# Kernel optimization log

Measured on AMD Instinct MI355X. Metric: run time of the kernel, lower is better.

Reference implementation:

```python
import jax, jax.numpy as jnp
import numpy as np

HID = 512
HEADS = 8
HD = HID // HEADS  # 64


def setup_inputs() -> dict:
    key = jax.random.key(0)
    ks = jax.random.split(key, 16)
    B, LQ, LK = 2, 384, 384
    s_in = 1.0 / np.sqrt(HID)
    s_hd = 1.0 / np.sqrt(HD)
    return {
        "query": jax.random.normal(ks[0], (B, LQ, HID), jnp.float32),
        "key":   jax.random.normal(ks[1], (B, LK, HID), jnp.float32),
        "value": jax.random.normal(ks[2], (B, LK, HID), jnp.float32),
        # linear weights stored as (in, out) so y = x @ W + b
        "Wq": jax.random.uniform(ks[3], (HID, HID), jnp.float32, -s_in, s_in),
        "bq": jnp.zeros((HID,), jnp.float32),
        "Wk": jax.random.uniform(ks[4], (HID, HID), jnp.float32, -s_in, s_in),
        "bk": jnp.zeros((HID,), jnp.float32),
        "Wv": jax.random.uniform(ks[5], (HID, HID), jnp.float32, -s_in, s_in),
        "bv": jnp.zeros((HID,), jnp.float32),
        "Ww": jax.random.uniform(ks[6], (HD, HD), jnp.float32, -s_hd, s_hd),
        "bw": jnp.zeros((HD,), jnp.float32),
        "Wu": jax.random.uniform(ks[7], (HD, HD), jnp.float32, -s_hd, s_hd),
        "bu": jnp.zeros((HD,), jnp.float32),
        "vv": jax.random.uniform(ks[8], (HD,), jnp.float32, -s_hd, s_hd),
        "Wo": jax.random.uniform(ks[9], (HID, HID), jnp.float32, -s_in, s_in),
        "bo": jnp.zeros((HID,), jnp.float32),
    }


def reference(query, key, value, Wq, bq, Wk, bk, Wv, bv, Ww, bw, Wu, bu, vv, Wo, bo):
    B, LQ, _ = query.shape
    LK = key.shape[1]
    scale = jnp.sqrt(jnp.asarray(HD, query.dtype))

    def split_heads(x, L):
        return x.reshape(B, L, HEADS, HD).transpose(0, 2, 1, 3)  # [B,H,L,hd]

    Q = split_heads(query @ Wq + bq, LQ)
    K = split_heads(key @ Wk + bk, LK)
    V = split_heads(value @ Wv + bv, LK)

    qW = Q @ Ww + bw            # [B,H,Lq,hd]
    kU = K @ Wu + bu            # [B,H,Lk,hd]
    # additive energy: tanh(W(Q)+U(K)) . vv  -> [B,H,Lq,Lk]
    e = jnp.tanh(qW[:, :, :, None, :] + kU[:, :, None, :, :])  # [B,H,Lq,Lk,hd]
    energy = jnp.einsum('bhqkd,d->bhqk', e, vv) / scale

    attention = jax.nn.softmax(energy, axis=-1)
    x = jnp.einsum('bhqk,bhkd->bhqd', attention, V)
    x = x.transpose(0, 2, 1, 3).reshape(B, LQ, HID)
    x = x @ Wo + bo
    return (x, attention)
```

## Files before the change

kernel.cpp:

```cpp
#include <hip/hip_runtime.h>

#define HID 512
#define HEADS 8
#define HD 64
#define BATCH 2
#define SEQ 384
#define MROWS (BATCH * SEQ)
#define KT_N 48
#define APACK_S8 (48 * KT_N * 64)
#define BPACK_S8 (32 * KT_N * 64)

#define C1 2.8853900817779268f
#define SSCL 0.18033688011112043f

typedef __attribute__((ext_vector_type(8))) short s8v;
typedef __attribute__((ext_vector_type(4))) float f4v;

__device__ __forceinline__ unsigned short bf16_rne(float x) {
    union { float f; unsigned u; } v; v.f = x;
    unsigned r = v.u + 0x7FFFu + ((v.u >> 16) & 1u);
    return (unsigned short)(r >> 16);
}
__device__ __forceinline__ float bf16_val(unsigned short h) {
    union { float f; unsigned u; } v; v.u = ((unsigned)h) << 16; return v.f;
}

__device__ __forceinline__ void pack_a_one(const float* __restrict__ src,
                                           s8v* __restrict__ dst, int rem)
{
    int g = rem & 63, m = rem >> 6;
    const float4* sp = (const float4*)(src + (size_t)m * HID + g * 8);
    float4 v0 = sp[0], v1 = sp[1];
    float vals[8] = {v0.x, v0.y, v0.z, v0.w, v1.x, v1.y, v1.z, v1.w};
    s8v hi, lo;
    #pragma unroll
    for (int j = 0; j < 8; ++j) {
        unsigned short h = bf16_rne(vals[j]);
        hi[j] = (short)h;
        lo[j] = (short)bf16_rne(vals[j] - bf16_val(h));
    }
    int mt = m >> 4, kt = g >> 2;
    int lanei = (m & 15) | ((g & 3) << 4);
    size_t base = ((size_t)mt * KT_N) * 64 + lanei;
    dst[base + (size_t)kt * 64]        = hi;
    dst[base + (size_t)(16 + kt) * 64] = hi;
    dst[base + (size_t)(32 + kt) * 64] = lo;
}

__device__ __forceinline__ void pack_w_store(s8v* __restrict__ dst,
                                             const float vals[8], int kg, int n)
{
    s8v hi, lo;
    #pragma unroll
    for (int j = 0; j < 8; ++j) {
        unsigned short h = bf16_rne(vals[j]);
        hi[j] = (short)h;
        lo[j] = (short)bf16_rne(vals[j] - bf16_val(h));
    }
    int nt = n >> 4, kt = kg >> 2;
    int lanei = (n & 15) | ((kg & 3) << 4);
    size_t base = ((size_t)nt * KT_N) * 64 + lanei;
    dst[base + (size_t)kt * 64]        = hi;
    dst[base + (size_t)(16 + kt) * 64] = lo;
    dst[base + (size_t)(32 + kt) * 64] = hi;
}

__device__ __forceinline__ void pack_w_one(const float* __restrict__ W,
                                           s8v* __restrict__ dst, int rem)
{
    int kg = rem >> 9, n = rem & 511;
    float vals[8];
    #pragma unroll
    for (int j = 0; j < 8; ++j)
        vals[j] = W[(size_t)(kg * 8 + j) * HID + n];
    pack_w_store(dst, vals, kg, n);
}

__device__ __forceinline__ void fold_pack_w_one(const float* __restrict__ Wbig,
                                                const float* __restrict__ Wsmall,
                                                s8v* __restrict__ dst, int rem)
{
    int kg = __builtin_amdgcn_readfirstlane(rem >> 9);
    int n  = rem & 511;
    int h  = __builtin_amdgcn_readfirstlane(n >> 6);
    int d  = n & 63;
    const float* wr = Wbig + (size_t)(kg * 8) * HID + h * HD;
    float acc[8] = {0.f, 0.f, 0.f, 0.f, 0.f, 0.f, 0.f, 0.f};
    #pragma unroll 8
    for (int t = 0; t < 64; ++t) {
        float wv = Wsmall[t * 64 + d];
        #pragma unroll
        for (int j = 0; j < 8; ++j)
            acc[j] = fmaf(wr[(size_t)j * HID + t], wv, acc[j]);
    }
    pack_w_store(dst, acc, kg, n);
}

__global__ __launch_bounds__(256) void pack_all_kernel(
    const float* __restrict__ q, const float* __restrict__ k, const float* __restrict__ v,
    const float* __restrict__ Wq, const float* __restrict__ bq,
    const float* __restrict__ Wk, const float* __restrict__ bk,
    const float* __restrict__ Wv, const float* __restrict__ Wo,
    const float* __restrict__ Ww, const float* __restrict__ bw,
    const float* __restrict__ Wu, const float* __restrict__ bu,
    const float* __restrict__ vv,
    s8v* __restrict__ Aq, s8v* __restrict__ Ak, s8v* __restrict__ Av,
    s8v* __restrict__ Bq, s8v* __restrict__ Bk, s8v* __restrict__ Bv, s8v* __restrict__ Bo,
    float* __restrict__ bqe, float* __restrict__ bke, float* __restrict__ vv2)
{
    int bx = blockIdx.x, tid = threadIdx.x;
    if (bx < 576) {
        int p = bx / 192;
        int rem = (bx % 192) * 256 + tid;
        const float* src = (p == 0) ? q : (p == 1) ? k : v;
        s8v* dst = (p == 0) ? Aq : (p == 1) ? Ak : Av;
        pack_a_one(src, dst, rem);
    } else if (bx < 704) {
        pack_w_one(Wv, Bv, (bx - 576) * 256 + tid);
    } else if (bx < 832) {
        pack_w_one(Wo, Bo, (bx - 704) * 256 + tid);
    } else if (bx < 960) {
        fold_pack_w_one(Wq, Ww, Bq, (bx - 832) * 256 + tid);
    } else if (bx < 1088) {
        fold_pack_w_one(Wk, Wu, Bk, (bx - 960) * 256 + tid);
    } else {
        for (int i = tid; i < 1088; i += 256) {
            if (i < 512) {
                int h = i >> 6, j = i & 63;
                float s = bw[j];
                for (int t = 0; t < 64; ++t) s = fmaf(bq[h * 64 + t], Ww[t * 64 + j], s);
                bqe[i] = s;
            } else if (i < 1024) {
                int n = i - 512, h = n >> 6, j = n & 63;
                float s = bu[j];
                for (int t = 0; t < 64; ++t) s = fmaf(bk[h * 64 + t], Wu[t * 64 + j], s);
                bke[n] = s;
            } else {
                vv2[i - 1024] = -2.0f * vv[i - 1024];
            }
        }
    }
}

template <int MODE>
__device__ __forceinline__ void mfma_gemm_body(
    const s8v* __restrict__ Ap, const s8v* __restrict__ Bp,
    const float* __restrict__ bias, float* __restrict__ out,
    int mt0, int nt0)
{
    int lane = threadIdx.x & 63;

    const s8v* a0p = Ap + (size_t)(mt0 * KT_N) * 64 + lane;
    const s8v* a1p = a0p + (size_t)KT_N * 64;
    const s8v* b0p = Bp + (size_t)(nt0 * KT_N) * 64 + lane;
    const s8v* b1p = b0p + (size_t)KT_N * 64;

    f4v acc00 = {0.f, 0.f, 0.f, 0.f};
    f4v acc01 = {0.f, 0.f, 0.f, 0.f};
    f4v acc10 = {0.f, 0.f, 0.f, 0.f};
    f4v acc11 = {0.f, 0.f, 0.f, 0.f};

    s8v xa0 = a0p[0], xa1 = a1p[0], xb0 = b0p[0], xb1 = b1p[0];
    #pragma unroll 1
    for (int kt = 0; kt < KT_N; kt += 2) {
        int o1 = (kt + 1) * 64;
        s8v ya0 = a0p[o1], ya1 = a1p[o1], yb0 = b0p[o1], yb1 = b1p[o1];
        acc00 = __builtin_amdgcn_mfma_f32_16x16x32_bf16(xa0, xb0, acc00, 0, 0, 0);
        acc01 = __builtin_amdgcn_mfma_f32_16x16x32_bf16(xa0, xb1, acc01, 0, 0, 0);
        acc10 = __builtin_amdgcn_mfma_f32_16x16x32_bf16(xa1, xb0, acc10, 0, 0, 0);
        acc11 = __builtin_amdgcn_mfma_f32_16x16x32_bf16(xa1, xb1, acc11, 0, 0, 0);
        int o2 = (kt + 2 < KT_N) ? (kt + 2) * 64 : 0;
        xa0 = a0p[o2]; xa1 = a1p[o2]; xb0 = b0p[o2]; xb1 = b1p[o2];
        acc00 = __builtin_amdgcn_mfma_f32_16x16x32_bf16(ya0, yb0, acc00, 0, 0, 0);
        acc01 = __builtin_amdgcn_mfma_f32_16x16x32_bf16(ya0, yb1, acc01, 0, 0, 0);
        acc10 = __builtin_amdgcn_mfma_f32_16x16x32_bf16(ya1, yb0, acc10, 0, 0, 0);
        acc11 = __builtin_amdgcn_mfma_f32_16x16x32_bf16(ya1, yb1, acc11, 0, 0, 0);
    }

    int quad = lane >> 4, c16 = lane & 15;
    int col0 = nt0 * 16 + c16, col1 = col0 + 16;
    float bias0 = bias[col0], bias1 = bias[col1];
    int row0 = mt0 * 16 + quad * 4;
    int row1 = row0 + 16;

    #pragma unroll
    for (int r = 0; r < 4; ++r) {
        float y;
        #define WR(ROW, COL, Y)                                                     \
        {                                                                           \
            float yy = (Y);                                                         \
            if (MODE != 0) yy = __builtin_amdgcn_exp2f(C1 * yy);                    \
            if (MODE == 2) {                                                        \
                int b2 = (ROW) / SEQ, kk = (ROW) - b2 * SEQ;                        \
                int hh = (COL) >> 6, dd = (COL) & 63;                               \
                out[(((size_t)((b2 * 8 + hh) * 16 + (dd >> 2)) * SEQ + kk) << 2)    \
                    + (dd & 3)] = yy;                                               \
            } else {                                                                \
                out[(size_t)(ROW) * HID + (COL)] = yy;                              \
            }                                                                       \
        }
        y = acc00[r] + bias0; WR(row0 + r, col0, y);
        y = acc01[r] + bias1; WR(row0 + r, col1, y);
        y = acc10[r] + bias0; WR(row1 + r, col0, y);
        y = acc11[r] + bias1; WR(row1 + r, col1, y);
        #undef WR
    }
}

__global__ __launch_bounds__(64) void proj3_mfma_kernel(
    const s8v* __restrict__ Aq, const s8v* __restrict__ Ak, const s8v* __restrict__ Av,
    const s8v* __restrict__ Bq, const s8v* __restrict__ Bk, const s8v* __restrict__ Bv,
    const float* __restrict__ bqe, const float* __restrict__ bke, const float* __restrict__ bv,
    float* __restrict__ Eq, float* __restrict__ Ek4, float* __restrict__ V)
{
    int p = blockIdx.z;
    int mt0 = blockIdx.x * 2, nt0 = blockIdx.y * 2;
    if (p == 0)      mfma_gemm_body<1>(Aq, Bq, bqe, Eq,  mt0, nt0);
    else if (p == 1) mfma_gemm_body<2>(Ak, Bk, bke, Ek4, mt0, nt0);
    else             mfma_gemm_body<0>(Av, Bv, bv,  V,   mt0, nt0);
}

__global__ __launch_bounds__(64) void out_mfma_kernel(
    const s8v* __restrict__ Ax, const s8v* __restrict__ Bo,
    const float* __restrict__ bo, float* __restrict__ out)
{
    mfma_gemm_body<0>(Ax, Bo, bo, out, blockIdx.x * 2, blockIdx.y * 2);
}

__global__ __launch_bounds__(256, 4) void attn_kernel(
    const float* __restrict__ Eq, const float* __restrict__ Ek4,
    const float* __restrict__ V, const float* __restrict__ vv2,
    float* __restrict__ attnOut, s8v* __restrict__ Ax)
{
    __shared__ float2 aP[4][SEQ];

    int bh = blockIdx.y;
    int b = bh >> 3, h = bh & 7;
    int tid = threadIdx.x;
    int wave = __builtin_amdgcn_readfirstlane(tid >> 6);
    int lane = tid & 63;
    int q0 = blockIdx.x * 8 + wave * 2, q1 = q0 + 1;

    const float* eq0 = Eq + (size_t)(b * SEQ + q0) * HID + h * HD;
    const float* eq1 = eq0 + HID;
    const float4* ekbase = (const float4*)Ek4 + (size_t)bh * 16 * SEQ + lane;

    float e0[6], e1[6];
    #pragma unroll
    for (int t = 0; t < 6; ++t) { e0[t] = 0.f; e1[t] = 0.f; }

    #pragma unroll 1
    for (int c = 0; c < 4; ++c) {
        float g0[16], g1[16], w[16];
        #pragma unroll
        for (int j = 0; j < 16; ++j) {
            g0[j] = eq0[c * 16 + j];
            g1[j] = eq1[c * 16 + j];
            w[j]  = vv2[c * 16 + j];
        }
        const float4* ekc = ekbase + (size_t)c * 4 * SEQ;
        float4 k0 = ekc[0 * SEQ], k1 = ekc[1 * SEQ];
        float4 k2 = ekc[2 * SEQ], k3 = ekc[3 * SEQ];
        #pragma unroll
        for (int kt = 0; kt < 6; ++kt) {
            float4 n0, n1, n2, n3;
            if (kt < 5) {
                const float4* np = ekc + (kt + 1) * 64;
                n0 = np[0 * SEQ]; n1 = np[1 * SEQ];
                n2 = np[2 * SEQ]; n3 = np[3 * SEQ];
            }
            float r0 = e0[kt], r1 = e1[kt];
            #define EN(J, KV)                                                      \
            {                                                                      \
                float t0 = __builtin_amdgcn_rcpf(fmaf(g0[J], (KV), 1.f));          \
                float t1 = __builtin_amdgcn_rcpf(fmaf(g1[J], (KV), 1.f));          \
                r0 = fmaf(w[J], t0, r0);                                           \
                r1 = fmaf(w[J], t1, r1);                                           \
            }
            EN(0,  k0.x) EN(1,  k0.y) EN(2,  k0.z) EN(3,  k0.w)
            EN(4,  k1.x) EN(5,  k1.y) EN(6,  k1.z) EN(7,  k1.w)
            EN(8,  k2.x) EN(9,  k2.y) EN(10, k2.z) EN(11, k2.w)
            EN(12, k3.x) EN(13, k3.y) EN(14, k3.z) EN(15, k3.w)
            #undef EN
            e0[kt] = r0; e1[kt] = r1;
            k0 = n0; k1 = n1; k2 = n2; k3 = n3;
        }
    }

    float m0 = e0[0], m1 = e1[0];
    #pragma unroll
    for (int t = 1; t < 6; ++t) { m0 = fmaxf(m0, e0[t]); m1 = fmaxf(m1, e1[t]); }
    #pragma unroll
    for (int off = 1; off < 64; off <<= 1) {
        m0 = fmaxf(m0, __shfl_xor(m0, off));
        m1 = fmaxf(m1, __shfl_xor(m1, off));
    }
    float a0[6], a1[6], s0 = 0.f, s1 = 0.f;
    #pragma unroll
    for (int t = 0; t < 6; ++t) {
        a0[t] = __builtin_amdgcn_exp2f((e0[t] - m0) * SSCL); s0 += a0[t];
        a1[t] = __builtin_amdgcn_exp2f((e1[t] - m1) * SSCL); s1 += a1[t];
    }
    #pragma unroll
    for (int off = 1; off < 64; off <<= 1) {
        s0 += __shfl_xor(s0, off);
        s1 += __shfl_xor(s1, off);
    }
    float z0 = __builtin_amdgcn_rcpf(s0), z1 = __builtin_amdgcn_rcpf(s1);

    size_t abase = (size_t)bh * SEQ * SEQ + (size_t)q0 * SEQ;
    #pragma unroll
    for (int t = 0; t < 6; ++t) {
        float v0 = a0[t] * z0, v1 = a1[t] * z1;
        attnOut[abase + t * 64 + lane] = v0;
        attnOut[abase + SEQ + t * 64 + lane] = v1;
        aP[wave][t * 64 + lane] = make_float2(v0, v1);
    }

    int ko = lane >> 4, d4p = lane & 15;
    const float4* vb = (const float4*)&V[(size_t)b * SEQ * HID + h * HD + d4p * 4];
    float4 x0 = make_float4(0.f, 0.f, 0.f, 0.f);
    float4 x1 = make_float4(0.f, 0.f, 0.f, 0.f);
    #pragma unroll 8
    for (int k = ko; k < SEQ; k += 4) {
        float4 v = vb[(size_t)k * (HID / 4)];
        float2 a = aP[wave][k];
        x0.x = fmaf(a.x, v.x, x0.x); x0.y = fmaf(a.x, v.y, x0.y);
        x0.z = fmaf(a.x, v.z, x0.z); x0.w = fmaf(a.x, v.w, x0.w);
        x1.x = fmaf(a.y, v.x, x1.x); x1.y = fmaf(a.y, v.y, x1.y);
        x1.z = fmaf(a.y, v.z, x1.z); x1.w = fmaf(a.y, v.w, x1.w);
    }
    #pragma unroll
    for (int off = 16; off < 64; off <<= 1) {
        x0.x += __shfl_xor(x0.x, off); x0.y += __shfl_xor(x0.y, off);
        x0.z += __shfl_xor(x0.z, off); x0.w += __shfl_xor(x0.w, off);
        x1.x += __shfl_xor(x1.x, off); x1.y += __shfl_xor(x1.y, off);
        x1.z += __shfl_xor(x1.z, off); x1.w += __shfl_xor(x1.w, off);
    }

    if (ko == 0) {
        float4 p0, p1;
        p0.x = __shfl_xor(x0.x, 1); p0.y = __shfl_xor(x0.y, 1);
        p0.z = __shfl_xor(x0.z, 1); p0.w = __shfl_xor(x0.w, 1);
        p1.x = __shfl_xor(x1.x, 1); p1.y = __shfl_xor(x1.y, 1);
        p1.z = __shfl_xor(x1.z, 1); p1.w = __shfl_xor(x1.w, 1);
        float vals[8];
        int row;
        if ((lane & 1) == 0) {
            vals[0] = x0.x; vals[1] = x0.y; vals[2] = x0.z; vals[3] = x0.w;
            vals[4] = p0.x; vals[5] = p0.y; vals[6] = p0.z; vals[7] = p0.w;
            row = b * SEQ + q0;
        } else {
            vals[0] = p1.x; vals[1] = p1.y; vals[2] = p1.z; vals[3] = p1.w;
            vals[4] = x1.x; vals[5] = x1.y; vals[6] = x1.z; vals[7] = x1.w;
            row = b * SEQ + q1;
        }
        int g = h * 8 + (lane >> 1);
        s8v hi, lo;
        #pragma unroll
        for (int j = 0; j < 8; ++j) {
            unsigned short hh = bf16_rne(vals[j]);
            hi[j] = (short)hh;
            lo[j] = (short)bf16_rne(vals[j] - bf16_val(hh));
        }
        int mt = row >> 4, kt2 = g >> 2;
        int lanei = (row & 15) | ((g & 3) << 4);
        size_t base = ((size_t)mt * KT_N) * 64 + lanei;
        Ax[base + (size_t)kt2 * 64]        = hi;
        Ax[base + (size_t)(16 + kt2) * 64] = hi;
        Ax[base + (size_t)(32 + kt2) * 64] = lo;
    }
}

extern "C" void kernel_launch(void* const* d_in, const int* in_sizes, int n_in,
                              void* d_out, int out_size, void* d_ws, size_t ws_size,
                              hipStream_t stream)
{
    const float* query = (const float*)d_in[0];
    const float* key   = (const float*)d_in[1];
    const float* value = (const float*)d_in[2];
    const float* Wq = (const float*)d_in[3];
    const float* bq = (const float*)d_in[4];
    const float* Wk = (const float*)d_in[5];
    const float* bk = (const float*)d_in[6];
    const float* Wv = (const float*)d_in[7];
    const float* bv = (const float*)d_in[8];
    const float* Ww = (const float*)d_in[9];
    const float* bw = (const float*)d_in[10];
    const float* Wu = (const float*)d_in[11];
    const float* bu = (const float*)d_in[12];
    const float* vv = (const float*)d_in[13];
    const float* Wo = (const float*)d_in[14];
    const float* bo = (const float*)d_in[15];

    float* out_x    = (float*)d_out;
    float* out_attn = out_x + (size_t)MROWS * HID;

    float* ws  = (float*)d_ws;
    float* bqe = ws;
    float* bke = bqe + 512;
    float* vv2 = bke + 512;
    float* EqB = vv2 + 64;
    float* Ek4 = EqB + 393216;
    float* Vw  = Ek4 + 393216;

    s8v* packs = (s8v*)(Vw + 393216);
    s8v* Aq = packs;
    s8v* Ak = Aq + APACK_S8;
    s8v* Av = Ak + APACK_S8;
    s8v* Ax = Av + APACK_S8;
    s8v* Bq = Ax + APACK_S8;
    s8v* Bk = Bq + BPACK_S8;
    s8v* Bv = Bk + BPACK_S8;
    s8v* Bo = Bv + BPACK_S8;

    pack_all_kernel<<<dim3(1089), 256, 0, stream>>>(
        query, key, value,
        Wq, bq, Wk, bk, Wv, Wo, Ww, bw, Wu, bu, vv,
        Aq, Ak, Av, Bq, Bk, Bv, Bo,
        bqe, bke, vv2);
    proj3_mfma_kernel<<<dim3(24, 16, 3), 64, 0, stream>>>(Aq, Ak, Av, Bq, Bk, Bv,
                                                          bqe, bke, bv,
                                                          EqB, Ek4, Vw);
    attn_kernel<<<dim3(48, 16), 256, 0, stream>>>(EqB, Ek4, Vw, vv2, out_attn, Ax);
    out_mfma_kernel<<<dim3(24, 16), 64, 0, stream>>>(Ax, Bo, bo, out_x);
}
```

Measured before the change: 148.0 us.

## Split attention key range across wave pairs with cross-wave softmax reduction

Each query pair is now handled by two waves that each cover half of the 384 keys, and the grid is doubled to 96x16 blocks. The row max, the row sum and the attention-times-V partial sums are combined across the two waves through shared memory and __syncthreads. Each wave holds fewer accumulators, and the launch bound is raised to 6 blocks per SM to allow more waves in flight. The cost is three block-wide barriers and some extra shared-memory traffic.

```diff
diff --git a/kernel.cpp b/kernel.cpp
--- a/kernel.cpp
+++ b/kernel.cpp
@@ -227,28 +227,31 @@
     mfma_gemm_body<0>(Ax, Bo, bo, out, blockIdx.x * 2, blockIdx.y * 2);
 }
 
-__global__ __launch_bounds__(256, 4) void attn_kernel(
+__global__ __launch_bounds__(256, 6) void attn_kernel(
     const float* __restrict__ Eq, const float* __restrict__ Ek4,
     const float* __restrict__ V, const float* __restrict__ vv2,
     float* __restrict__ attnOut, s8v* __restrict__ Ax)
 {
-    __shared__ float2 aP[4][SEQ];
+    __shared__ float2 aP[2][SEQ];
+    __shared__ float  red[2][2][2][2];
+    __shared__ float4 xred[2][2][16];
 
     int bh = blockIdx.y;
     int b = bh >> 3, h = bh & 7;
     int tid = threadIdx.x;
     int wave = __builtin_amdgcn_readfirstlane(tid >> 6);
     int lane = tid & 63;
-    int q0 = blockIdx.x * 8 + wave * 2, q1 = q0 + 1;
+    int pair = wave >> 1, khalf = wave & 1;
+    int q0 = blockIdx.x * 4 + pair * 2, q1 = q0 + 1;
 
     const float* eq0 = Eq + (size_t)(b * SEQ + q0) * HID + h * HD;
     const float* eq1 = eq0 + HID;
-    const float4* ekbase = (const float4*)Ek4 + (size_t)bh * 16 * SEQ + lane;
-
-    float e0[6], e1[6];
-    #pragma unroll
-    for (int t = 0; t < 6; ++t) { e0[t] = 0.f; e1[t] = 0.f; }
-
+    const float4* ekbase = (const float4*)Ek4 + (size_t)bh * 16 * SEQ
+                         + khalf * 3 * 64 + lane;
+
+    float e0[3] = {0.f, 0.f, 0.f}, e1[3] = {0.f, 0.f, 0.f};
+
+    float4 k0 = ekbase[0], k1 = ekbase[SEQ], k2 = ekbase[2 * SEQ], k3 = ekbase[3 * SEQ];
     #pragma unroll 1
     for (int c = 0; c < 4; ++c) {
         float g0[16], g1[16], w[16];
@@ -258,16 +261,13 @@
             g1[j] = eq1[c * 16 + j];
             w[j]  = vv2[c * 16 + j];
         }
-        const float4* ekc = ekbase + (size_t)c * 4 * SEQ;
-        float4 k0 = ekc[0 * SEQ], k1 = ekc[1 * SEQ];
-        float4 k2 = ekc[2 * SEQ], k3 = ekc[3 * SEQ];
         #pragma unroll
-        for (int kt = 0; kt < 6; ++kt) {
+        for (int kt = 0; kt < 3; ++kt) {
             float4 n0, n1, n2, n3;
-            if (kt < 5) {
-                const float4* np = ekc + (kt + 1) * 64;
-                n0 = np[0 * SEQ]; n1 = np[1 * SEQ];
-                n2 = np[2 * SEQ]; n3 = np[3 * SEQ];
+            if (!(c == 3 && kt == 2)) {
+                const float4* np = (kt < 2) ? (ekbase + c * 4 * SEQ + (kt + 1) * 64)
+                                            : (ekbase + (c + 1) * 4 * SEQ);
+                n0 = np[0]; n1 = np[SEQ]; n2 = np[2 * SEQ]; n3 = np[3 * SEQ];
             }
             float r0 = e0[kt], r1 = e1[kt];
             #define EN(J, KV)                                                      \
@@ -287,17 +287,21 @@
         }
     }
 
-    float m0 = e0[0], m1 = e1[0];
-    #pragma unroll
-    for (int t = 1; t < 6; ++t) { m0 = fmaxf(m0, e0[t]); m1 = fmaxf(m1, e1[t]); }
+    float m0 = fmaxf(fmaxf(e0[0], e0[1]), e0[2]);
+    float m1 = fmaxf(fmaxf(e1[0], e1[1]), e1[2]);
     #pragma unroll
     for (int off = 1; off < 64; off <<= 1) {
         m0 = fmaxf(m0, __shfl_xor(m0, off));
         m1 = fmaxf(m1, __shfl_xor(m1, off));
     }
-    float a0[6], a1[6], s0 = 0.f, s1 = 0.f;
-    #pragma unroll
-    for (int t = 0; t < 6; ++t) {
+    if (lane == 0) { red[0][pair][0][khalf] = m0; red[0][pair][1][khalf] = m1; }
+    __syncthreads();
+    m0 = fmaxf(red[0][pair][0][0], red[0][pair][0][1]);
+    m1 = fmaxf(red[0][pair][1][0], red[0][pair][1][1]);
+
+    float a0[3], a1[3], s0 = 0.f, s1 = 0.f;
+    #pragma unroll
+    for (int t = 0; t < 3; ++t) {
         a0[t] = __builtin_amdgcn_exp2f((e0[t] - m0) * SSCL); s0 += a0[t];
         a1[t] = __builtin_amdgcn_exp2f((e1[t] - m1) * SSCL); s1 += a1[t];
     }
@@ -306,25 +310,30 @@
         s0 += __shfl_xor(s0, off);
         s1 += __shfl_xor(s1, off);
     }
+    if (lane == 0) { red[1][pair][0][khalf] = s0; red[1][pair][1][khalf] = s1; }
+    __syncthreads();
+    s0 = red[1][pair][0][0] + red[1][pair][0][1];
+    s1 = red[1][pair][1][0] + red[1][pair][1][1];
     float z0 = __builtin_amdgcn_rcpf(s0), z1 = __builtin_amdgcn_rcpf(s1);
 
-    size_t abase = (size_t)bh * SEQ * SEQ + (size_t)q0 * SEQ;
-    #pragma unroll
-    for (int t = 0; t < 6; ++t) {
+    size_t abase = (size_t)bh * SEQ * SEQ + (size_t)q0 * SEQ + khalf * 192;
+    #pragma unroll
+    for (int t = 0; t < 3; ++t) {
         float v0 = a0[t] * z0, v1 = a1[t] * z1;
         attnOut[abase + t * 64 + lane] = v0;
         attnOut[abase + SEQ + t * 64 + lane] = v1;
-        aP[wave][t * 64 + lane] = make_float2(v0, v1);
+        aP[pair][khalf * 192 + t * 64 + lane] = make_float2(v0, v1);
     }
 
     int ko = lane >> 4, d4p = lane & 15;
     const float4* vb = (const float4*)&V[(size_t)b * SEQ * HID + h * HD + d4p * 4];
     float4 x0 = make_float4(0.f, 0.f, 0.f, 0.f);
     float4 x1 = make_float4(0.f, 0.f, 0.f, 0.f);
+    int kend = khalf * 192 + 192;
     #pragma unroll 8
-    for (int k = ko; k < SEQ; k += 4) {
+    for (int k = khalf * 192 + ko; k < kend; k += 4) {
         float4 v = vb[(size_t)k * (HID / 4)];
-        float2 a = aP[wave][k];
+        float2 a = aP[pair][k];
         x0.x = fmaf(a.x, v.x, x0.x); x0.y = fmaf(a.x, v.y, x0.y);
         x0.z = fmaf(a.x, v.z, x0.z); x0.w = fmaf(a.x, v.w, x0.w);
         x1.x = fmaf(a.y, v.x, x1.x); x1.y = fmaf(a.y, v.y, x1.y);
@@ -337,8 +346,17 @@
         x1.x += __shfl_xor(x1.x, off); x1.y += __shfl_xor(x1.y, off);
         x1.z += __shfl_xor(x1.z, off); x1.w += __shfl_xor(x1.w, off);
     }
-
-    if (ko == 0) {
+    if (khalf == 1 && ko == 0) {
+        xred[pair][0][d4p] = x0;
+        xred[pair][1][d4p] = x1;
+    }
+    __syncthreads();
+
+    if (khalf == 0 && ko == 0) {
+        float4 o0 = xred[pair][0][d4p], o1 = xred[pair][1][d4p];
+        x0.x += o0.x; x0.y += o0.y; x0.z += o0.z; x0.w += o0.w;
+        x1.x += o1.x; x1.y += o1.y; x1.z += o1.z; x1.w += o1.w;
+
         float4 p0, p1;
         p0.x = __shfl_xor(x0.x, 1); p0.y = __shfl_xor(x0.y, 1);
         p0.z = __shfl_xor(x0.z, 1); p0.w = __shfl_xor(x0.w, 1);
@@ -422,6 +440,6 @@
     proj3_mfma_kernel<<<dim3(24, 16, 3), 64, 0, stream>>>(Aq, Ak, Av, Bq, Bk, Bv,
                                                           bqe, bke, bv,
                                                           EqB, Ek4, Vw);
-    attn_kernel<<<dim3(48, 16), 256, 0, stream>>>(EqB, Ek4, Vw, vv2, out_attn, Ax);
+    attn_kernel<<<dim3(96, 16), 256, 0, stream>>>(EqB, Ek4, Vw, vv2, out_attn, Ax);
     out_mfma_kernel<<<dim3(24, 16), 64, 0, stream>>>(Ax, Bo, bo, out_x);
 }
```

Result: slower. 217.6 us (+47.0%).
